# Optimization experiments

Hardware: AMD Instinct MI355X
Metric: run time of the kernel (lower is better)

The kernel has to match this reference:

```python
import jax, jax.numpy as jnp
import numpy as np

M = 6            # num posenc frequencies
K0 = -3
WIDTH = 128
DEPTH = 7
N_PTS = 131072
N_ANNEAL = 0.6 * 5000.0   # self.N = 0.6 * max_iter
PI = 3.14                 # module uses literal 3.14, not math.pi


def _linear_init(key, fan_in, fan_out):
    k1, k2 = jax.random.split(key)
    lim = 1.0 / np.sqrt(fan_in)
    W = jax.random.uniform(k1, (fan_out, fan_in), jnp.float32, -lim, lim)
    b = jax.random.uniform(k2, (fan_out,), jnp.float32, -lim, lim)
    return W, b


def setup_inputs() -> dict:
    key = jax.random.key(0)
    ks = jax.random.split(key, 11)
    dim_x = M * 6 + 3  # 39
    W_in, b_in = _linear_init(ks[0], dim_x, WIDTH)
    hw, hb = [], []
    for i in range(DEPTH - 1):
        W, b = _linear_init(ks[1 + i], WIDTH, WIDTH)
        hw.append(W)
        hb.append(b)
    Ws, bs = jnp.stack(hw), jnp.stack(hb)  # [6,128,128], [6,128]
    Ww, bw = _linear_init(ks[7], WIDTH, 3)
    Wv, bv = _linear_init(ks[8], WIDTH, 3)
    x = jax.random.normal(ks[9], (N_PTS, 3), jnp.float32)
    return {"x": x, "W_in": W_in, "b_in": b_in, "Ws": Ws, "bs": bs,
            "Ww": Ww, "bw": bw, "Wv": Wv, "bv": bv, "iter": 2500}


def _posenc(pos, it):
    # pos: [N,3]
    j = jnp.arange(M, dtype=pos.dtype)
    a = M * it / N_ANNEAL
    w_a = (1.0 - jnp.cos(jnp.clip(a - j, 0.0, 1.0) * PI)) * 0.5      # [M]
    mul = (2.0 ** (j + K0)) * PI                                     # [M]
    ang = pos[..., :, None] * mul                                    # [N,3,M]
    sin = jnp.sin(ang) * w_a
    cos = jnp.cos(ang) * w_a
    # order: sinx,cosx,siny,cosy,sinz,cosz -> [N,3,2,M] flattened
    code = jnp.stack([sin, cos], axis=-2).reshape(pos.shape[0], 6 * M)
    return jnp.concatenate([pos, code], axis=-1)                     # [N,3+6M]


def _skew(w):
    z = jnp.zeros_like(w[..., 0])
    return jnp.stack([
        jnp.stack([z, -w[..., 2], w[..., 1]], -1),
        jnp.stack([w[..., 2], z, -w[..., 0]], -1),
        jnp.stack([-w[..., 1], w[..., 0], z], -1)], -2)              # [N,3,3]


def _exp_se3(w, v, theta):
    # w,v: [N,3] (axis and v/theta), theta: [N,1]
    W = _skew(w)
    W2 = W @ W
    th = theta[..., None]                                            # [N,1,1]
    s, c = jnp.sin(th), jnp.cos(th)
    I = jnp.eye(3, dtype=w.dtype)
    R = I + s * W + (1.0 - c) * W2
    G = I * th + (1.0 - c) * W + (th - s) * W2
    t = G @ v[..., None]                                             # [N,3,1]
    return R, t


def _warp(x, it, W_in, b_in, Ws, bs, Ww, bw, Wv, bv):
    fea = _posenc(x, it)
    fea = jax.nn.leaky_relu(fea @ W_in.T + b_in, 0.01)

    def layer(f, Wb):
        W, b = Wb
        return jax.nn.relu(f @ W.T + b), None

    fea, _ = jax.lax.scan(layer, fea, (Ws, bs))
    w = fea @ Ww.T + bw
    v = fea @ Wv.T + bv
    theta = jnp.linalg.norm(w, axis=-1, keepdims=True)
    w = w / theta
    v = v / theta
    R, t = _exp_se3(w, v, theta)
    return (R @ x[..., None] + t)[..., 0]                            # [N,3]


def reference(x, W_in, b_in, Ws, bs, Ww, bw, Wv, bv, iter):
    it = float(iter)
    warped = _warp(x, it, W_in, b_in, Ws, bs, Ww, bw, Wv, bv)
    # jacobian of sum over batch -> [3, N, 3]; transpose -> [N, 3, 3]
    f_sum = lambda xx: _warp(xx, it, W_in, b_in, Ws, bs, Ww, bw, Wv, bv).sum(0)
    J = jnp.transpose(jax.jacrev(f_sum)(x), (1, 0, 2))
    return warped, J
```

## Files before the change

kernel.cpp:

```cpp
#include <hip/hip_runtime.h>
#include <math.h>

#define NPTS    131072
#define PPB     32
#define THREADS 256
#define NBLK    (NPTS / PPB)
#define HOFF    (7 * 16384)
#define HSZ     (32 * 128)

typedef __attribute__((ext_vector_type(8)))  short short8;
typedef __attribute__((ext_vector_type(16))) float f32x16;
typedef __attribute__((ext_vector_type(2)))  short s16x2;
typedef __attribute__((ext_vector_type(2)))  __bf16 bf16x2v;

union b8cv { short8 v; unsigned u[4]; };

__device__ __forceinline__ unsigned short f2bf(float f) {
  unsigned u = __float_as_uint(f);
  unsigned r = (u + 0x7fffu + ((u >> 16) & 1u)) >> 16;
  return (unsigned short)r;
}
__device__ __forceinline__ unsigned pk2(float lo, float hi) {
  bf16x2v t;
  t[0] = (__bf16)lo;
  t[1] = (__bf16)hi;
  unsigned u; __builtin_memcpy(&u, &t, 4); return u;
}
__device__ __forceinline__ void gld16(const unsigned short* g, unsigned short* l) {
  __builtin_amdgcn_global_load_lds(
      (const __attribute__((address_space(1))) unsigned int*)(g),
      (__attribute__((address_space(3))) unsigned int*)(l), 16, 0, 0);
}
__device__ __forceinline__ float qbcast0(float v) {
  return __int_as_float(
      __builtin_amdgcn_mov_dpp(__float_as_int(v), 0x000, 0xf, 0xf, true));
}
__device__ __forceinline__ unsigned relu_pk(unsigned p) {
  unsigned vs = (unsigned)__builtin_amdgcn_mov_dpp((int)p, 0x000, 0xf, 0xf, true);
  s16x2 m2; __builtin_memcpy(&m2, &vs, 4);
  m2 = m2 >> 15;
  unsigned m; __builtin_memcpy(&m, &m2, 4);
  unsigned r;
  asm("v_bfi_b32 %0, %1, 0, %2" : "=v"(r) : "v"(m), "v"(p));
  return r;
}
__device__ __forceinline__ void cross3(const float a[3], const float b[3], float o[3]) {
  o[0] = a[1]*b[2] - a[2]*b[1];
  o[1] = a[2]*b[0] - a[0]*b[2];
  o[2] = a[0]*b[1] - a[1]*b[0];
}
__device__ __forceinline__ float dot3(const float a[3], const float b[3]) {
  return a[0]*b[0] + a[1]*b[1] + a[2]*b[2];
}

__global__ void convert_weights(const float* __restrict__ W_in,
                                const float* __restrict__ b_in,
                                const float* __restrict__ Ws,
                                const float* __restrict__ bs,
                                const float* __restrict__ Ww,
                                const float* __restrict__ Wv,
                                unsigned short* __restrict__ wsW) {
  int idx = blockIdx.x * 256 + threadIdx.x;
  if (idx >= HOFF + HSZ) return;
  float v;
  if (idx < HOFF) {
    int l = idx >> 14, r = idx & 16383, c = r >> 7, k = r & 127;
    if (l == 0) {
      if (k < 39) {
        v = W_in[c * 39 + k];
      } else if (k >= 64 && c < 14) {
        int j  = c * 64 + (k - 64);
        int lb = j >> 7, rr = j & 127;
        int mt = rr >> 5, rd = rr & 31;
        int e2 = rd & 3, hh = (rd >> 2) & 1, q = rd >> 3;
        int src = 32*mt + 16*(q>>1) + 8*hh + 4*(q&1) + e2;
        v = (lb == 0) ? b_in[src] : bs[(lb - 1) * 128 + src];
      } else {
        v = 0.0f;
      }
    } else {
      v = Ws[(l - 1) * 16384 + c * 128 + k];
    }
  } else {
    int r = idx - HOFF, o = r >> 7, k = r & 127;
    v = (o < 3) ? Ww[o * 128 + k] : (o < 6) ? Wv[(o - 3) * 128 + k] : 0.0f;
  }
  wsW[idx] = f2bf(v);
}

__device__ __forceinline__ void dma_half(const unsigned short* __restrict__ g,
                                         unsigned short* lds, int tid) {
  #pragma unroll
  for (int i = 0; i < 4; ++i) {
    int flat = i * 256 + tid;
    int R = flat >> 4, chs = flat & 15, ch = chs ^ (R & 15);
    gld16(g + R * 128 + ch * 8, lds + flat * 8);
  }
}

__device__ __forceinline__ short8 bias_af(const unsigned short* __restrict__ bb,
                                          int off, int c32) {
  b8cv cv;
  cv.u[0] = (unsigned)bb[off + c32];
  cv.u[1] = 0; cv.u[2] = 0; cv.u[3] = 0;
  return cv.v;
}

template <int NKS, bool LEAKY, bool HASNEXT>
__device__ __forceinline__ void mlp_layer(short8 (&pregv)[8],
                                          unsigned short* s0, unsigned short* s1,
                                          const unsigned short* s0s,
                                          const unsigned short* s1s,
                                          const int (&aoff)[8],
                                          const unsigned short* __restrict__ bb,
                                          const short8 bind, const f32x16& Z,
                                          const unsigned short* __restrict__ Wthis,
                                          const unsigned short* __restrict__ Wnext,
                                          int h, int tid, int c32) {
  dma_half(Wthis + 64 * 128, s1, tid);

  short8 tmp[4];

  {
    f32x16 acc[2];
    acc[0] = __builtin_amdgcn_mfma_f32_32x32x16_bf16(bias_af(bb,  64, c32), bind, Z, 0, 0, 0);
    acc[1] = __builtin_amdgcn_mfma_f32_32x32x16_bf16(bias_af(bb,  96, c32), bind, Z, 0, 0, 0);
    #pragma unroll
    for (int ks = 0; ks < NKS; ++ks) {
      #pragma unroll
      for (int m = 0; m < 2; ++m) {
        short8 af = *(const short8*)(s0s + m * 4096 + aoff[ks]);
        acc[m] = __builtin_amdgcn_mfma_f32_32x32x16_bf16(af, pregv[ks], acc[m], 0, 0, 0);
      }
    }
    #pragma unroll
    for (int mt = 0; mt < 2; ++mt)
      #pragma unroll
      for (int qh = 0; qh < 2; ++qh) {
        b8cv cv;
        #pragma unroll
        for (int qs = 0; qs < 2; ++qs) {
          int q = 2*qh + qs;
          if (LEAKY) {
            float pr[4];
            #pragma unroll
            for (int e2 = 0; e2 < 4; ++e2) {
              float post = acc[mt][4*q + e2];
              float vraw = qbcast0(post);
              pr[e2] = vraw > 0.0f ? post : post * 0.01f;
            }
            cv.u[2*qs]     = pk2(pr[0], pr[1]);
            cv.u[2*qs + 1] = pk2(pr[2], pr[3]);
          } else {
            cv.u[2*qs]     = relu_pk(pk2(acc[mt][4*q+0], acc[mt][4*q+1]));
            cv.u[2*qs + 1] = relu_pk(pk2(acc[mt][4*q+2], acc[mt][4*q+3]));
          }
        }
        tmp[2*mt + qh] = cv.v;
      }
  }

  __syncthreads();
  if (HASNEXT) dma_half(Wnext, s0, tid);

  {
    f32x16 acc[2];
    acc[0] = __builtin_amdgcn_mfma_f32_32x32x16_bf16(bias_af(bb, 192, c32), bind, Z, 0, 0, 0);
    acc[1] = __builtin_amdgcn_mfma_f32_32x32x16_bf16(bias_af(bb, 224, c32), bind, Z, 0, 0, 0);
    #pragma unroll
    for (int ks = 0; ks < NKS; ++ks) {
      #pragma unroll
      for (int m = 0; m < 2; ++m) {
        short8 af = *(const short8*)(s1s + m * 4096 + aoff[ks]);
        acc[m] = __builtin_amdgcn_mfma_f32_32x32x16_bf16(af, pregv[ks], acc[m], 0, 0, 0);
      }
    }
    #pragma unroll
    for (int mt = 0; mt < 2; ++mt)
      #pragma unroll
      for (int qh = 0; qh < 2; ++qh) {
        b8cv cv;
        #pragma unroll
        for (int qs = 0; qs < 2; ++qs) {
          int q = 2*qh + qs;
          if (LEAKY) {
            float pr[4];
            #pragma unroll
            for (int e2 = 0; e2 < 4; ++e2) {
              float post = acc[mt][4*q + e2];
              float vraw = qbcast0(post);
              pr[e2] = vraw > 0.0f ? post : post * 0.01f;
            }
            cv.u[2*qs]     = pk2(pr[0], pr[1]);
            cv.u[2*qs + 1] = pk2(pr[2], pr[3]);
          } else {
            cv.u[2*qs]     = relu_pk(pk2(acc[mt][4*q+0], acc[mt][4*q+1]));
            cv.u[2*qs + 1] = relu_pk(pk2(acc[mt][4*q+2], acc[mt][4*q+3]));
          }
        }
        pregv[4 + 2*mt + qh] = cv.v;
      }
  }

  #pragma unroll
  for (int i = 0; i < 4; ++i) pregv[i] = tmp[i];
  __syncthreads();
}

__global__ __launch_bounds__(THREADS, 4)
void nerfies_mfma(const float* __restrict__ x,
                  const float* __restrict__ bw,
                  const float* __restrict__ bv,
                  const unsigned short* __restrict__ wsW,
                  const int* __restrict__ iterp,
                  float* __restrict__ out)
{
  __shared__ __align__(16) unsigned short sWl[2][64 * 128];
  float* sH = (float*)sWl[1];

  const int tid  = threadIdx.x;
  const int lane = tid & 63;
  const int wv   = tid >> 6;
  const int c32  = lane & 31;
  const int h    = lane >> 5;
  const int p0   = blockIdx.x * PPB;
  const int sig  = (c32 & 0x13) | ((c32 & 4) << 1) | ((c32 & 8) >> 1);

  dma_half(wsW, sWl[0], tid);

  int aoff[8];
  #pragma unroll
  for (int ks = 0; ks < 8; ++ks) aoff[ks] = ((2*ks + h) ^ (sig & 15)) << 3;
  const unsigned short* s0s = sWl[0] + sig * 128;
  const unsigned short* s1s = sWl[1] + sig * 128;

  f32x16 Z;
  #pragma unroll
  for (int e = 0; e < 16; ++e) Z[e] = 0.0f;
  short8 bind;
  {
    b8cv cv;
    cv.u[0] = ((c32 & 3) == 0) ? 0x3F00u : 0u;
    cv.u[1] = 0; cv.u[2] = 0; cv.u[3] = 0;
    bind = cv.v;
  }

  const int d  = c32 & 3;
  const int gp = p0 + wv * 8 + (c32 >> 2);
  float X[3] = { x[gp * 3 + 0], x[gp * 3 + 1], x[gp * 3 + 2] };

  int iraw = iterp[0];
  float it = (iraw > 0 && iraw < 100000000) ? (float)iraw : ((const float*)iterp)[0];
  const float aM = 6.0f * it / 3000.0f;

  short8 pregv[8];
  #pragma unroll
  for (int j = 4; j < 8; ++j) pregv[j] = (short8)0;
  #pragma unroll
  for (int j = 0; j < 4; ++j) {
    b8cv cv;
    #pragma unroll
    for (int ii = 0; ii < 4; ++ii) {
      int i = 4*j + ii;
      int mt = i >> 3, rr = i & 7, q = rr >> 1, s = rr & 1;
      int u0 = 32*mt + 16*(q>>1) + 8*h + 4*(q&1) + 2*s;
      float vp[2];
      #pragma unroll
      for (int ci = 0; ci < 2; ++ci) {
        int c = u0 + ci;
        float val = 0.0f;
        if (c < 3) {
          val = (d == 0) ? X[c] : ((c == d - 1) ? 1.0f : 0.0f);
        } else if (c < 39) {
          int kk = c - 3;
          int a  = kk / 12;
          int rm = kk - a * 12;
          int t  = rm / 6;
          int jf = rm - t * 6;
          float e2 = exp2f((float)(jf - 3));
          float mj = e2 * 3.14f;
          float tt = fminf(fmaxf(aM - (float)jf, 0.0f), 1.0f);
          float wj = (1.0f - __builtin_amdgcn_cosf(tt * 0.49974652f)) * 0.5f;
          float rev = X[a] * (e2 * 0.49974652f);
          float fr  = rev - floorf(rev);
          float sv = __builtin_amdgcn_sinf(fr);
          float cvv = __builtin_amdgcn_cosf(fr);
          if (d == 0)          val = (t == 0 ? sv : cvv) * wj;
          else if (a == d - 1) val = (t == 0 ? cvv : -sv) * (mj * wj);
        }
        vp[ci] = val;
      }
      cv.u[ii] = pk2(vp[0], vp[1]);
    }
    pregv[j] = cv.v;
  }
  __syncthreads();

  mlp_layer<3, true , true >(pregv, sWl[0], sWl[1], s0s, s1s, aoff, wsW + 0*256, bind, Z, wsW + 0*16384, wsW + 1*16384, h, tid, c32);
  mlp_layer<8, false, true >(pregv, sWl[0], sWl[1], s0s, s1s, aoff, wsW + 1*256, bind, Z, wsW + 1*16384, wsW + 2*16384, h, tid, c32);
  mlp_layer<8, false, true >(pregv, sWl[0], sWl[1], s0s, s1s, aoff, wsW + 2*256, bind, Z, wsW + 2*16384, wsW + 3*16384, h, tid, c32);
  mlp_layer<8, false, true >(pregv, sWl[0], sWl[1], s0s, s1s, aoff, wsW + 3*256, bind, Z, wsW + 3*16384, wsW + 4*16384, h, tid, c32);
  mlp_layer<8, false, true >(pregv, sWl[0], sWl[1], s0s, s1s, aoff, wsW + 4*256, bind, Z, wsW + 4*16384, wsW + 5*16384, h, tid, c32);
  mlp_layer<8, false, true >(pregv, sWl[0], sWl[1], s0s, s1s, aoff, wsW + 5*256, bind, Z, wsW + 5*16384, wsW + 6*16384, h, tid, c32);
  mlp_layer<8, false, false>(pregv, sWl[0], sWl[1], s0s, s1s, aoff, wsW + 6*256, bind, Z, wsW + 6*16384, wsW,           h, tid, c32);

  {
    const unsigned short* hw = wsW + HOFF;
    short8 af0 = *(const short8*)(hw + c32 * 128 + 8 * h);
    f32x16 hacc = __builtin_amdgcn_mfma_f32_32x32x16_bf16(af0, pregv[0], Z, 0, 0, 0);
    #pragma unroll
    for (int ks = 1; ks < 8; ++ks) {
      short8 afrag = *(const short8*)(hw + c32 * 128 + ks * 16 + 8 * h);
      hacc = __builtin_amdgcn_mfma_f32_32x32x16_bf16(afrag, pregv[ks], hacc, 0, 0, 0);
    }
    int rg = wv * 32 + c32;
    if (h == 0) {
      *(float4*)(sH + rg * 8) = make_float4(hacc[0], hacc[1], hacc[2], hacc[3]);
    } else {
      *(float2*)(sH + rg * 8 + 4) = make_float2(hacc[0], hacc[1]);
    }
  }
  __syncthreads();

  if (lane < 8) {
    const int p  = wv * 8 + lane;
    const int gpp = p0 + p;
    float XX[3] = { x[gpp*3+0], x[gpp*3+1], x[gpp*3+2] };
    float w[3], v[3], dw[3][3], dv[3][3];
    const int rb = p * 4;
    #pragma unroll
    for (int i = 0; i < 3; ++i) {
      w[i] = sH[rb * 8 + i]     + bw[i];
      v[i] = sH[rb * 8 + 3 + i] + bv[i];
      #pragma unroll
      for (int dd = 0; dd < 3; ++dd) {
        dw[dd][i] = sH[(rb + 1 + dd) * 8 + i];
        dv[dd][i] = sH[(rb + 1 + dd) * 8 + 3 + i];
      }
    }
    float th  = sqrtf(w[0]*w[0] + w[1]*w[1] + w[2]*w[2]);
    float ith = 1.0f / th;
    float u[3]  = { w[0]*ith, w[1]*ith, w[2]*ith };
    float vh[3] = { v[0]*ith, v[1]*ith, v[2]*ith };
    float s = sinf(th), c = cosf(th);
    float C2 = 1.0f - c;
    float ths = th - s;
    float uxx[3]; cross3(u, XX, uxx);
    float udx = dot3(u, XX);
    float uxv[3]; cross3(u, vh, uxv);
    float udv = dot3(u, vh);
    #pragma unroll
    for (int i = 0; i < 3; ++i) {
      float Rx = XX[i] + s * uxx[i] + C2 * (u[i] * udx - XX[i]);
      float tt = th * vh[i] + C2 * uxv[i] + ths * (u[i] * udv - vh[i]);
      out[gpp*3 + i] = Rx + tt;
    }
    float* Jout = out + (size_t)NPTS * 3 + (size_t)gpp * 9;
    #pragma unroll
    for (int dd = 0; dd < 3; ++dd) {
      float dwv[3] = { dw[dd][0], dw[dd][1], dw[dd][2] };
      float dvv[3] = { dv[dd][0], dv[dd][1], dv[dd][2] };
      float dth = dot3(w, dwv) * ith;
      float du[3], dvhv[3];
      #pragma unroll
      for (int i = 0; i < 3; ++i) {
        du[i]   = (dwv[i] - u[i]  * dth) * ith;
        dvhv[i] = (dvv[i] - vh[i] * dth) * ith;
      }
      float ex[3] = { dd == 0 ? 1.0f : 0.0f, dd == 1 ? 1.0f : 0.0f, dd == 2 ? 1.0f : 0.0f };
      float dsv  = c  * dth;
      float dC2  = s  * dth;
      float dths = C2 * dth;
      float duxx[3]; cross3(du, XX, duxx);
      float uxe[3];  cross3(u, ex, uxe);
      float dudx = dot3(du, XX) + u[dd];
      float duxv[3]; cross3(du, vh, duxv);
      float uxdv[3]; cross3(u, dvhv, uxdv);
      float dudv = dot3(du, vh) + dot3(u, dvhv);
      #pragma unroll
      for (int i = 0; i < 3; ++i) {
        float dRx = ex[i] + dsv * uxx[i] + s * (duxx[i] + uxe[i])
                  + dC2 * (u[i] * udx - XX[i])
                  + C2 * (du[i] * udx + u[i] * dudx - ex[i]);
        float dt  = dth * vh[i] + th * dvhv[i] + dC2 * uxv[i]
                  + C2 * (duxv[i] + uxdv[i])
                  + dths * (u[i] * udv - vh[i])
                  + ths * (du[i] * udv + u[i] * dudv - dvhv[i]);
        Jout[i * 3 + dd] = dRx + dt;
      }
    }
  }
}

extern "C" void kernel_launch(void* const* d_in, const int* in_sizes, int n_in,
                              void* d_out, int out_size, void* d_ws, size_t ws_size,
                              hipStream_t stream) {
  const float* x    = (const float*)d_in[0];
  const float* W_in = (const float*)d_in[1];
  const float* b_in = (const float*)d_in[2];
  const float* Ws   = (const float*)d_in[3];
  const float* bs   = (const float*)d_in[4];
  const float* Ww   = (const float*)d_in[5];
  const float* bw   = (const float*)d_in[6];
  const float* Wv   = (const float*)d_in[7];
  const float* bv   = (const float*)d_in[8];
  const int*   itp  = (const int*)d_in[9];
  unsigned short* wsW = (unsigned short*)d_ws;

  convert_weights<<<dim3((HOFF + HSZ + 255) / 256), dim3(256), 0, stream>>>(
      W_in, b_in, Ws, bs, Ww, Wv, wsW);
  nerfies_mfma<<<dim3(NBLK), dim3(THREADS), 0, stream>>>(
      x, bw, bv, wsW, itp, (float*)d_out);
}
```

Before: 206.2 us.

## Process two point groups per wave to reuse each LDS weight fragment

Each block now handles 64 points instead of 32. Every wave carries two independent activation register sets (A and B) through all MLP layers, so each weight fragment read from LDS feeds two MFMAs. This halves the weight DMA and LDS reads per point and gives the scheduler independent MFMA chains to interleave. The cost is roughly double the accumulator and activation registers, so launch bounds drop from 4 to 2 blocks per CU, which lowers occupancy and leaves half as many blocks.

```diff
diff --git a/kernel.cpp b/kernel.cpp
--- a/kernel.cpp
+++ b/kernel.cpp
@@ -2,7 +2,7 @@
 #include <math.h>
 
 #define NPTS    131072
-#define PPB     32
+#define PPB     64
 #define THREADS 256
 #define NBLK    (NPTS / PPB)
 #define HOFF    (7 * 16384)
@@ -106,156 +106,104 @@
   return cv.v;
 }
 
+template <bool LEAKY>
+__device__ __forceinline__ void act_pack(const f32x16 (&acc)[2], short8* dst) {
+  #pragma unroll
+  for (int mt = 0; mt < 2; ++mt)
+    #pragma unroll
+    for (int qh = 0; qh < 2; ++qh) {
+      b8cv cv;
+      #pragma unroll
+      for (int qs = 0; qs < 2; ++qs) {
+        int q = 2*qh + qs;
+        if (LEAKY) {
+          float pr[4];
+          #pragma unroll
+          for (int e2 = 0; e2 < 4; ++e2) {
+            float post = acc[mt][4*q + e2];
+            float vraw = qbcast0(post);
+            pr[e2] = vraw > 0.0f ? post : post * 0.01f;
+          }
+          cv.u[2*qs]     = pk2(pr[0], pr[1]);
+          cv.u[2*qs + 1] = pk2(pr[2], pr[3]);
+        } else {
+          cv.u[2*qs]     = relu_pk(pk2(acc[mt][4*q+0], acc[mt][4*q+1]));
+          cv.u[2*qs + 1] = relu_pk(pk2(acc[mt][4*q+2], acc[mt][4*q+3]));
+        }
+      }
+      dst[2*mt + qh] = cv.v;
+    }
+}
+
 template <int NKS, bool LEAKY, bool HASNEXT>
-__device__ __forceinline__ void mlp_layer(short8 (&pregv)[8],
-                                          unsigned short* s0, unsigned short* s1,
+__device__ __forceinline__ void mlp_layer(short8 (&pgA)[8], short8 (&pgB)[8],
                                           const unsigned short* s0s,
                                           const unsigned short* s1s,
+                                          unsigned short* s0w, unsigned short* s1w,
                                           const int (&aoff)[8],
                                           const unsigned short* __restrict__ bb,
                                           const short8 bind, const f32x16& Z,
                                           const unsigned short* __restrict__ Wthis,
                                           const unsigned short* __restrict__ Wnext,
-                                          int h, int tid, int c32) {
-  dma_half(Wthis + 64 * 128, s1, tid);
-
-  short8 tmp[4];
+                                          int tid, int c32) {
+  dma_half(Wthis + 64 * 128, s1w, tid);
+
+  short8 tA[4], tB[4];
 
   {
-    f32x16 acc[2];
-    acc[0] = __builtin_amdgcn_mfma_f32_32x32x16_bf16(bias_af(bb,  64, c32), bind, Z, 0, 0, 0);
-    acc[1] = __builtin_amdgcn_mfma_f32_32x32x16_bf16(bias_af(bb,  96, c32), bind, Z, 0, 0, 0);
+    f32x16 aA[2], aB[2];
+    short8 bf0 = bias_af(bb,  64, c32);
+    short8 bf1 = bias_af(bb,  96, c32);
+    aA[0] = __builtin_amdgcn_mfma_f32_32x32x16_bf16(bf0, bind, Z, 0, 0, 0);
+    aB[0] = __builtin_amdgcn_mfma_f32_32x32x16_bf16(bf0, bind, Z, 0, 0, 0);
+    aA[1] = __builtin_amdgcn_mfma_f32_32x32x16_bf16(bf1, bind, Z, 0, 0, 0);
+    aB[1] = __builtin_amdgcn_mfma_f32_32x32x16_bf16(bf1, bind, Z, 0, 0, 0);
     #pragma unroll
     for (int ks = 0; ks < NKS; ++ks) {
       #pragma unroll
       for (int m = 0; m < 2; ++m) {
         short8 af = *(const short8*)(s0s + m * 4096 + aoff[ks]);
-        acc[m] = __builtin_amdgcn_mfma_f32_32x32x16_bf16(af, pregv[ks], acc[m], 0, 0, 0);
-      }
-    }
-    #pragma unroll
-    for (int mt = 0; mt < 2; ++mt)
-      #pragma unroll
-      for (int qh = 0; qh < 2; ++qh) {
-        b8cv cv;
-        #pragma unroll
-        for (int qs = 0; qs < 2; ++qs) {
-          int q = 2*qh + qs;
-          if (LEAKY) {
-            float pr[4];
-            #pragma unroll
-            for (int e2 = 0; e2 < 4; ++e2) {
-              float post = acc[mt][4*q + e2];
-              float vraw = qbcast0(post);
-              pr[e2] = vraw > 0.0f ? post : post * 0.01f;
-            }
-            cv.u[2*qs]     = pk2(pr[0], pr[1]);
-            cv.u[2*qs + 1] = pk2(pr[2], pr[3]);
-          } else {
-            cv.u[2*qs]     = relu_pk(pk2(acc[mt][4*q+0], acc[mt][4*q+1]));
-            cv.u[2*qs + 1] = relu_pk(pk2(acc[mt][4*q+2], acc[mt][4*q+3]));
-          }
-        }
-        tmp[2*mt + qh] = cv.v;
-      }
+        aA[m] = __builtin_amdgcn_mfma_f32_32x32x16_bf16(af, pgA[ks], aA[m], 0, 0, 0);
+        aB[m] = __builtin_amdgcn_mfma_f32_32x32x16_bf16(af, pgB[ks], aB[m], 0, 0, 0);
+      }
+    }
+    act_pack<LEAKY>(aA, tA);
+    act_pack<LEAKY>(aB, tB);
   }
 
   __syncthreads();
-  if (HASNEXT) dma_half(Wnext, s0, tid);
+  if (HASNEXT) dma_half(Wnext, s0w, tid);
 
   {
-    f32x16 acc[2];
-    acc[0] = __builtin_amdgcn_mfma_f32_32x32x16_bf16(bias_af(bb, 192, c32), bind, Z, 0, 0, 0);
-    acc[1] = __builtin_amdgcn_mfma_f32_32x32x16_bf16(bias_af(bb, 224, c32), bind, Z, 0, 0, 0);
+    f32x16 aA[2], aB[2];
+    short8 bf2 = bias_af(bb, 192, c32);
+    short8 bf3 = bias_af(bb, 224, c32);
+    aA[0] = __builtin_amdgcn_mfma_f32_32x32x16_bf16(bf2, bind, Z, 0, 0, 0);
+    aB[0] = __builtin_amdgcn_mfma_f32_32x32x16_bf16(bf2, bind, Z, 0, 0, 0);
+    aA[1] = __builtin_amdgcn_mfma_f32_32x32x16_bf16(bf3, bind, Z, 0, 0, 0);
+    aB[1] = __builtin_amdgcn_mfma_f32_32x32x16_bf16(bf3, bind, Z, 0, 0, 0);
     #pragma unroll
     for (int ks = 0; ks < NKS; ++ks) {
       #pragma unroll
       for (int m = 0; m < 2; ++m) {
         short8 af = *(const short8*)(s1s + m * 4096 + aoff[ks]);
-        acc[m] = __builtin_amdgcn_mfma_f32_32x32x16_bf16(af, pregv[ks], acc[m], 0, 0, 0);
-      }
-    }
-    #pragma unroll
-    for (int mt = 0; mt < 2; ++mt)
-      #pragma unroll
-      for (int qh = 0; qh < 2; ++qh) {
-        b8cv cv;
-        #pragma unroll
-        for (int qs = 0; qs < 2; ++qs) {
-          int q = 2*qh + qs;
-          if (LEAKY) {
-            float pr[4];
-            #pragma unroll
-            for (int e2 = 0; e2 < 4; ++e2) {
-              float post = acc[mt][4*q + e2];
-              float vraw = qbcast0(post);
-              pr[e2] = vraw > 0.0f ? post : post * 0.01f;
-            }
-            cv.u[2*qs]     = pk2(pr[0], pr[1]);
-            cv.u[2*qs + 1] = pk2(pr[2], pr[3]);
-          } else {
-            cv.u[2*qs]     = relu_pk(pk2(acc[mt][4*q+0], acc[mt][4*q+1]));
-            cv.u[2*qs + 1] = relu_pk(pk2(acc[mt][4*q+2], acc[mt][4*q+3]));
-          }
-        }
-        pregv[4 + 2*mt + qh] = cv.v;
-      }
-  }
-
-  #pragma unroll
-  for (int i = 0; i < 4; ++i) pregv[i] = tmp[i];
+        aA[m] = __builtin_amdgcn_mfma_f32_32x32x16_bf16(af, pgA[ks], aA[m], 0, 0, 0);
+        aB[m] = __builtin_amdgcn_mfma_f32_32x32x16_bf16(af, pgB[ks], aB[m], 0, 0, 0);
+      }
+    }
+    act_pack<LEAKY>(aA, &pgA[4]);
+    act_pack<LEAKY>(aB, &pgB[4]);
+  }
+
+  #pragma unroll
+  for (int i = 0; i < 4; ++i) { pgA[i] = tA[i]; pgB[i] = tB[i]; }
   __syncthreads();
 }
 
-__global__ __launch_bounds__(THREADS, 4)
-void nerfies_mfma(const float* __restrict__ x,
-                  const float* __restrict__ bw,
-                  const float* __restrict__ bv,
-                  const unsigned short* __restrict__ wsW,
-                  const int* __restrict__ iterp,
-                  float* __restrict__ out)
-{
-  __shared__ __align__(16) unsigned short sWl[2][64 * 128];
-  float* sH = (float*)sWl[1];
-
-  const int tid  = threadIdx.x;
-  const int lane = tid & 63;
-  const int wv   = tid >> 6;
-  const int c32  = lane & 31;
-  const int h    = lane >> 5;
-  const int p0   = blockIdx.x * PPB;
-  const int sig  = (c32 & 0x13) | ((c32 & 4) << 1) | ((c32 & 8) >> 1);
-
-  dma_half(wsW, sWl[0], tid);
-
-  int aoff[8];
-  #pragma unroll
-  for (int ks = 0; ks < 8; ++ks) aoff[ks] = ((2*ks + h) ^ (sig & 15)) << 3;
-  const unsigned short* s0s = sWl[0] + sig * 128;
-  const unsigned short* s1s = sWl[1] + sig * 128;
-
-  f32x16 Z;
-  #pragma unroll
-  for (int e = 0; e < 16; ++e) Z[e] = 0.0f;
-  short8 bind;
-  {
-    b8cv cv;
-    cv.u[0] = ((c32 & 3) == 0) ? 0x3F00u : 0u;
-    cv.u[1] = 0; cv.u[2] = 0; cv.u[3] = 0;
-    bind = cv.v;
-  }
-
-  const int d  = c32 & 3;
-  const int gp = p0 + wv * 8 + (c32 >> 2);
-  float X[3] = { x[gp * 3 + 0], x[gp * 3 + 1], x[gp * 3 + 2] };
-
-  int iraw = iterp[0];
-  float it = (iraw > 0 && iraw < 100000000) ? (float)iraw : ((const float*)iterp)[0];
-  const float aM = 6.0f * it / 3000.0f;
-
-  short8 pregv[8];
-  #pragma unroll
-  for (int j = 4; j < 8; ++j) pregv[j] = (short8)0;
+__device__ __forceinline__ void posenc_pack(const float X[3], int d, int h,
+                                            float aM, short8* pg) {
+  #pragma unroll
+  for (int j = 4; j < 8; ++j) pg[j] = (short8)0;
   #pragma unroll
   for (int j = 0; j < 4; ++j) {
     b8cv cv;
@@ -292,42 +240,101 @@
       }
       cv.u[ii] = pk2(vp[0], vp[1]);
     }
-    pregv[j] = cv.v;
-  }
+    pg[j] = cv.v;
+  }
+}
+
+__global__ __launch_bounds__(THREADS, 2)
+void nerfies_mfma(const float* __restrict__ x,
+                  const float* __restrict__ bw,
+                  const float* __restrict__ bv,
+                  const unsigned short* __restrict__ wsW,
+                  const int* __restrict__ iterp,
+                  float* __restrict__ out)
+{
+  __shared__ __align__(16) unsigned short sWl[2][64 * 128];
+  float* sH = (float*)sWl[1];
+
+  const int tid  = threadIdx.x;
+  const int lane = tid & 63;
+  const int wv   = tid >> 6;
+  const int c32  = lane & 31;
+  const int h    = lane >> 5;
+  const int p0   = blockIdx.x * PPB;
+  const int sig  = (c32 & 0x13) | ((c32 & 4) << 1) | ((c32 & 8) >> 1);
+
+  dma_half(wsW, sWl[0], tid);
+
+  int aoff[8];
+  #pragma unroll
+  for (int ks = 0; ks < 8; ++ks) aoff[ks] = ((2*ks + h) ^ (sig & 15)) << 3;
+  const unsigned short* s0s = sWl[0] + sig * 128;
+  const unsigned short* s1s = sWl[1] + sig * 128;
+
+  f32x16 Z;
+  #pragma unroll
+  for (int e = 0; e < 16; ++e) Z[e] = 0.0f;
+  short8 bind;
+  {
+    b8cv cv;
+    cv.u[0] = ((c32 & 3) == 0) ? 0x3F00u : 0u;
+    cv.u[1] = 0; cv.u[2] = 0; cv.u[3] = 0;
+    bind = cv.v;
+  }
+
+  const int d   = c32 & 3;
+  const int gpA = p0 + wv * 16 + (c32 >> 2);
+  const int gpB = gpA + 8;
+  float XA[3] = { x[gpA * 3 + 0], x[gpA * 3 + 1], x[gpA * 3 + 2] };
+  float XB[3] = { x[gpB * 3 + 0], x[gpB * 3 + 1], x[gpB * 3 + 2] };
+
+  int iraw = iterp[0];
+  float it = (iraw > 0 && iraw < 100000000) ? (float)iraw : ((const float*)iterp)[0];
+  const float aM = 6.0f * it / 3000.0f;
+
+  short8 pgA[8], pgB[8];
+  posenc_pack(XA, d, h, aM, pgA);
+  posenc_pack(XB, d, h, aM, pgB);
   __syncthreads();
 
-  mlp_layer<3, true , true >(pregv, sWl[0], sWl[1], s0s, s1s, aoff, wsW + 0*256, bind, Z, wsW + 0*16384, wsW + 1*16384, h, tid, c32);
-  mlp_layer<8, false, true >(pregv, sWl[0], sWl[1], s0s, s1s, aoff, wsW + 1*256, bind, Z, wsW + 1*16384, wsW + 2*16384, h, tid, c32);
-  mlp_layer<8, false, true >(pregv, sWl[0], sWl[1], s0s, s1s, aoff, wsW + 2*256, bind, Z, wsW + 2*16384, wsW + 3*16384, h, tid, c32);
-  mlp_layer<8, false, true >(pregv, sWl[0], sWl[1], s0s, s1s, aoff, wsW + 3*256, bind, Z, wsW + 3*16384, wsW + 4*16384, h, tid, c32);
-  mlp_layer<8, false, true >(pregv, sWl[0], sWl[1], s0s, s1s, aoff, wsW + 4*256, bind, Z, wsW + 4*16384, wsW + 5*16384, h, tid, c32);
-  mlp_layer<8, false, true >(pregv, sWl[0], sWl[1], s0s, s1s, aoff, wsW + 5*256, bind, Z, wsW + 5*16384, wsW + 6*16384, h, tid, c32);
-  mlp_layer<8, false, false>(pregv, sWl[0], sWl[1], s0s, s1s, aoff, wsW + 6*256, bind, Z, wsW + 6*16384, wsW,           h, tid, c32);
+  mlp_layer<3, true , true >(pgA, pgB, s0s, s1s, sWl[0], sWl[1], aoff, wsW + 0*256, bind, Z, wsW + 0*16384, wsW + 1*16384, tid, c32);
+  mlp_layer<8, false, true >(pgA, pgB, s0s, s1s, sWl[0], sWl[1], aoff, wsW + 1*256, bind, Z, wsW + 1*16384, wsW + 2*16384, tid, c32);
+  mlp_layer<8, false, true >(pgA, pgB, s0s, s1s, sWl[0], sWl[1], aoff, wsW + 2*256, bind, Z, wsW + 2*16384, wsW + 3*16384, tid, c32);
+  mlp_layer<8, false, true >(pgA, pgB, s0s, s1s, sWl[0], sWl[1], aoff, wsW + 3*256, bind, Z, wsW + 3*16384, wsW + 4*16384, tid, c32);
+  mlp_layer<8, false, true >(pgA, pgB, s0s, s1s, sWl[0], sWl[1], aoff, wsW + 4*256, bind, Z, wsW + 4*16384, wsW + 5*16384, tid, c32);
+  mlp_layer<8, false, true >(pgA, pgB, s0s, s1s, sWl[0], sWl[1], aoff, wsW + 5*256, bind, Z, wsW + 5*16384, wsW + 6*16384, tid, c32);
+  mlp_layer<8, false, false>(pgA, pgB, s0s, s1s, sWl[0], sWl[1], aoff, wsW + 6*256, bind, Z, wsW + 6*16384, wsW,           tid, c32);
 
   {
     const unsigned short* hw = wsW + HOFF;
     short8 af0 = *(const short8*)(hw + c32 * 128 + 8 * h);
-    f32x16 hacc = __builtin_amdgcn_mfma_f32_32x32x16_bf16(af0, pregv[0], Z, 0, 0, 0);
+    f32x16 hA = __builtin_amdgcn_mfma_f32_32x32x16_bf16(af0, pgA[0], Z, 0, 0, 0);
+    f32x16 hB = __builtin_amdgcn_mfma_f32_32x32x16_bf16(af0, pgB[0], Z, 0, 0, 0);
     #pragma unroll
     for (int ks = 1; ks < 8; ++ks) {
       short8 afrag = *(const short8*)(hw + c32 * 128 + ks * 16 + 8 * h);
-      hacc = __builtin_amdgcn_mfma_f32_32x32x16_bf16(afrag, pregv[ks], hacc, 0, 0, 0);
-    }
-    int rg = wv * 32 + c32;
+      hA = __builtin_amdgcn_mfma_f32_32x32x16_bf16(afrag, pgA[ks], hA, 0, 0, 0);
+      hB = __builtin_amdgcn_mfma_f32_32x32x16_bf16(afrag, pgB[ks], hB, 0, 0, 0);
+    }
+    int rgA = wv * 64 + c32;
+    int rgB = rgA + 32;
     if (h == 0) {
-      *(float4*)(sH + rg * 8) = make_float4(hacc[0], hacc[1], hacc[2], hacc[3]);
+      *(float4*)(sH + rgA * 8) = make_float4(hA[0], hA[1], hA[2], hA[3]);
+      *(float4*)(sH + rgB * 8) = make_float4(hB[0], hB[1], hB[2], hB[3]);
     } else {
-      *(float2*)(sH + rg * 8 + 4) = make_float2(hacc[0], hacc[1]);
+      *(float2*)(sH + rgA * 8 + 4) = make_float2(hA[0], hA[1]);
+      *(float2*)(sH + rgB * 8 + 4) = make_float2(hB[0], hB[1]);
     }
   }
   __syncthreads();
 
-  if (lane < 8) {
-    const int p  = wv * 8 + lane;
-    const int gpp = p0 + p;
+  if (lane < 16) {
+    const int p   = lane;
+    const int g   = p >> 3, pi = p & 7;
+    const int gpp = p0 + wv * 16 + p;
+    const int rb  = wv * 64 + g * 32 + pi * 4;
     float XX[3] = { x[gpp*3+0], x[gpp*3+1], x[gpp*3+2] };
     float w[3], v[3], dw[3][3], dv[3][3];
-    const int rb = p * 4;
     #pragma unroll
     for (int i = 0; i < 3; ++i) {
       w[i] = sH[rb * 8 + i]     + bw[i];
```

Measured after the change: 186.6 us. -9.5%, faster.
